# Performance work log

Measured on AMD Instinct MI355X. Metric: run time of the kernel, lower is better.

The kernel has to match this reference:

```python
import jax, jax.numpy as jnp
import numpy as np

NUM_EMB = 1024
EMB_DIM = 256
BETA = 0.25


def setup_inputs() -> dict:
    key = jax.random.key(0)
    k1, k2 = jax.random.split(key)
    z_e = jax.random.normal(k1, (32, EMB_DIM, 32, 32), dtype=jnp.float32)
    # original inits uniform(-1/num_emb, 1/num_emb)
    emb_weight = jax.random.uniform(k2, (NUM_EMB, EMB_DIM), dtype=jnp.float32,
                                    minval=-1.0 / NUM_EMB, maxval=1.0 / NUM_EMB)
    return {"z_e": z_e, "emb_weight": emb_weight}


def reference(z_e, emb_weight):
    # (B, C, H, W) -> (B, H, W, C)
    z = jnp.transpose(z_e, (0, 2, 3, 1))
    B, H, W, C = z.shape
    z_flat = z.reshape(-1, C)  # (N, C)
    # squared L2 distances to codebook: ||z||^2 + ||e||^2 - 2 z e^T
    d = (jnp.sum(z_flat ** 2, axis=1, keepdims=True)
         + jnp.sum(emb_weight ** 2, axis=1)
         - 2.0 * jnp.matmul(z_flat, emb_weight.T))  # (N, num_emb)
    encoding_indices = jnp.argmin(d, axis=1)  # (N,)
    # one-hot matmul == gather of codebook rows
    z_q = jnp.take(emb_weight, encoding_indices, axis=0).reshape(B, H, W, C)
    # vq losses
    L_e = jnp.mean((jax.lax.stop_gradient(z_q) - z) ** 2)
    L_q = jnp.mean((z_q - jax.lax.stop_gradient(z)) ** 2)
    vq_loss = L_e + BETA * L_q
    # straight-through estimator
    z_q_st = z + jax.lax.stop_gradient(z_q - z)
    z_q_out = jnp.transpose(z_q_st, (0, 3, 1, 2))  # (B, C, H, W)
    return z_q_out, vq_loss, encoding_indices
```

## Files before the change

kernel.cpp:

```cpp
#include <hip/hip_runtime.h>

#define NUM_EMB 1024
#define EMB_DIM 256
#define NPIX    32768
#define HW      1024
#define ZQ_ELEMS 8388608

#define WS_TNORM 8
#define WS_SNORM 8192
#define WS_KEYS  139264
#define WS_CNT   401408
#define WS_EPL   401424
#define EPLANE_ELEMS (NUM_EMB * EMB_DIM)

typedef unsigned long long u64;
typedef unsigned int u32;
typedef unsigned short u16;

typedef __bf16 bf16x8 __attribute__((ext_vector_type(8)));
typedef float f32x16 __attribute__((ext_vector_type(16)));
typedef u16 u16x8 __attribute__((ext_vector_type(8)));

__device__ __forceinline__ float pw128_sq(const float* x, int stride) {
  float r[8];
#pragma unroll
  for (int j = 0; j < 8; ++j) {
    float v = x[(size_t)j * stride];
    r[j] = __fmul_rn(v, v);
  }
  for (int i = 8; i < 128; i += 8) {
#pragma unroll
    for (int j = 0; j < 8; ++j) {
      float v = x[(size_t)(i + j) * stride];
      r[j] = __fadd_rn(r[j], __fmul_rn(v, v));
    }
  }
  float s01 = __fadd_rn(r[0], r[1]);
  float s23 = __fadd_rn(r[2], r[3]);
  float s45 = __fadd_rn(r[4], r[5]);
  float s67 = __fadd_rn(r[6], r[7]);
  return __fadd_rn(__fadd_rn(s01, s23), __fadd_rn(s45, s67));
}

__device__ __forceinline__ void split3(float x, u16& h, u16& m, u16& l) {
  u32 u = __float_as_uint(x);
  u16 hb = (u16)((u + 0x7fffu + ((u >> 16) & 1u)) >> 16);
  float hf = __uint_as_float((u32)hb << 16);
  float r1 = x - hf;
  u32 u1 = __float_as_uint(r1);
  u16 mb = (u16)((u1 + 0x7fffu + ((u1 >> 16) & 1u)) >> 16);
  float mf = __uint_as_float((u32)mb << 16);
  float r2 = r1 - mf;
  u32 u2 = __float_as_uint(r2);
  u16 lb = (u16)((u2 + 0x7fffu + ((u2 >> 16) & 1u)) >> 16);
  h = hb; m = mb; l = lb;
}

__device__ __forceinline__ u64 shfl_xor_u64(u64 v, int msk) {
  const u32 lo = __shfl_xor((u32)v, msk, 64);
  const u32 hi = __shfl_xor((u32)(v >> 32), msk, 64);
  return ((u64)hi << 32) | lo;
}

__global__ __launch_bounds__(256) void vq_prep_kernel(
    const float* __restrict__ z, const float* __restrict__ emb,
    float* __restrict__ tnorm, float* __restrict__ snorm,
    unsigned long long* __restrict__ keys, double* __restrict__ loss_accum,
    u32* __restrict__ counter,
    u16* __restrict__ eh, u16* __restrict__ em, u16* __restrict__ el) {
  const int gid = blockIdx.x * 256 + threadIdx.x;
  if (gid == 0) *loss_accum = 0.0;
  if (gid == 1) *counter = 0u;
  if (gid < NPIX) {
    keys[gid] = ~0ull;
    const int b = gid >> 10, hw = gid & 1023;
    const float* base = z + (size_t)b * (EMB_DIM * HW) + hw;
    snorm[gid] = __fadd_rn(pw128_sq(base, HW), pw128_sq(base + (size_t)128 * HW, HW));
  } else {
    const int k = gid - NPIX;
    if (k < NUM_EMB) {
      const float* row = emb + (size_t)k * EMB_DIM;
      tnorm[k] = __fadd_rn(pw128_sq(row, 1), pw128_sq(row + 128, 1));
      for (int c = 0; c < EMB_DIM; c += 8) {
        u16x8 vh, vm, vl;
#pragma unroll
        for (int j = 0; j < 8; ++j) {
          u16 h_, m_, l_;
          split3(row[c + j], h_, m_, l_);
          vh[j] = h_; vm[j] = m_; vl[j] = l_;
        }
        *(u16x8*)(eh + (size_t)k * EMB_DIM + c) = vh;
        *(u16x8*)(em + (size_t)k * EMB_DIM + c) = vm;
        *(u16x8*)(el + (size_t)k * EMB_DIM + c) = vl;
      }
    }
  }
}

__global__ __launch_bounds__(256, 2) void vq_main_kernel(
    const float* __restrict__ z,
    const u16* __restrict__ eh, const u16* __restrict__ em,
    const u16* __restrict__ el,
    const float* __restrict__ tnorm, const float* __restrict__ snorm,
    unsigned long long* __restrict__ keys) {
  __shared__ __align__(16) u16 zs[3][128][40];

  const int t   = threadIdx.x;
  const int hb  = blockIdx.x;
  const int bid = (hb & 7) * 256 + (hb >> 3);
  const int pt  = bid >> 3;
  const int ntb = bid & 7;
  const int m0  = pt * 128;
  const int n0  = ntb * 128;
  const int b   = m0 >> 10;
  const int hw0 = m0 & 1023;
  const float* zbase = z + (size_t)b * (EMB_DIM * HW) + hw0;

  const int l    = t & 63;
  const int wid  = t >> 6;
  const int wpx0 = (wid >> 1) * 64;
  const int wcb  = (wid & 1) * 64;
  const int cl   = l & 31;
  const int hi   = l >> 5;

  const int spx = t & 127;
  const int skh = (t >> 7) * 16;

  const u16* eplan[3] = {eh, em, el};
  size_t ebase[2];
  ebase[0] = (size_t)(n0 + wcb + cl) * EMB_DIM + (size_t)hi * 8;
  ebase[1] = (size_t)(n0 + wcb + 32 + cl) * EMB_DIM + (size_t)hi * 8;

  float gz[16];
#pragma unroll
  for (int j = 0; j < 16; ++j)
    gz[j] = zbase[(size_t)(skh + j) * HW + spx];

  f32x16 acc[2][2];
#pragma unroll
  for (int i = 0; i < 2; ++i)
#pragma unroll
    for (int j = 0; j < 2; ++j)
#pragma unroll
      for (int r = 0; r < 16; ++r) acc[i][j][r] = 0.0f;

  for (int kt = 0; kt < 8; ++kt) {
#pragma unroll
    for (int c = 0; c < 2; ++c) {
      u16x8 vh, vm, vl;
#pragma unroll
      for (int j = 0; j < 8; ++j) {
        u16 h_, m_, l_;
        split3(gz[c * 8 + j], h_, m_, l_);
        vh[j] = h_; vm[j] = m_; vl[j] = l_;
      }
      *(u16x8*)&zs[0][spx][skh + c * 8] = vh;
      *(u16x8*)&zs[1][spx][skh + c * 8] = vm;
      *(u16x8*)&zs[2][spx][skh + c * 8] = vl;
    }
    if (kt < 7) {
      const int kb = (kt + 1) * 32;
#pragma unroll
      for (int j = 0; j < 16; ++j)
        gz[j] = zbase[(size_t)(kb + skh + j) * HW + spx];
    }
    bf16x8 ge[3][2][2];
#pragma unroll
    for (int p = 0; p < 3; ++p)
#pragma unroll
      for (int nn = 0; nn < 2; ++nn)
#pragma unroll
        for (int ks = 0; ks < 2; ++ks)
          ge[p][nn][ks] =
              *(const bf16x8*)(eplan[p] + ebase[nn] + (size_t)kt * 32 + ks * 16);
    __syncthreads();

#pragma unroll
    for (int ks = 0; ks < 2; ++ks) {
      bf16x8 af[3][2];
#pragma unroll
      for (int p = 0; p < 3; ++p)
#pragma unroll
        for (int mt = 0; mt < 2; ++mt)
          af[p][mt] =
              *(const bf16x8*)&zs[p][wpx0 + mt * 32 + cl][ks * 16 + hi * 8];
#define PROD(PA, PB)                                                          \
      _Pragma("unroll")                                                       \
      for (int mt = 0; mt < 2; ++mt) {                                        \
        _Pragma("unroll")                                                     \
        for (int nn = 0; nn < 2; ++nn)                                        \
          acc[mt][nn] = __builtin_amdgcn_mfma_f32_32x32x16_bf16(              \
              af[PA][mt], ge[PB][nn][ks], acc[mt][nn], 0, 0, 0);              \
      }
      PROD(0, 0)
      PROD(0, 1)
      PROD(1, 0)
      PROD(1, 1)
      PROD(0, 2)
      PROD(2, 0)
#undef PROD
    }
    __syncthreads();
  }

  const float tv0 = tnorm[n0 + wcb + cl];
  const float tv1 = tnorm[n0 + wcb + 32 + cl];
  u64 bk[2][16];
#pragma unroll
  for (int mt = 0; mt < 2; ++mt)
#pragma unroll
    for (int reg = 0; reg < 16; ++reg) {
      const int row = wpx0 + mt * 32 + (reg & 3) + 8 * (reg >> 2) + 4 * hi;
      const float s = snorm[m0 + row];
      const float d0 = __fsub_rn(__fadd_rn(s, tv0), 2.0f * acc[mt][0][reg]);
      const float d1 = __fsub_rn(__fadd_rn(s, tv1), 2.0f * acc[mt][1][reg]);
      const u64 k0 = ((u64)__float_as_uint(d0) << 32) | (u32)(n0 + wcb + cl);
      const u64 k1 =
          ((u64)__float_as_uint(d1) << 32) | (u32)(n0 + wcb + 32 + cl);
      bk[mt][reg] = k0 < k1 ? k0 : k1;
    }
#pragma unroll
  for (int off = 1; off < 32; off <<= 1) {
#pragma unroll
    for (int mt = 0; mt < 2; ++mt)
#pragma unroll
      for (int reg = 0; reg < 16; ++reg) {
        const u64 o = shfl_xor_u64(bk[mt][reg], off);
        if (o < bk[mt][reg]) bk[mt][reg] = o;
      }
  }

  u64* part = (u64*)&zs[0][0][0];
  if (cl == 0) {
#pragma unroll
    for (int mt = 0; mt < 2; ++mt)
#pragma unroll
      for (int reg = 0; reg < 16; ++reg) {
        const int row = wpx0 + mt * 32 + (reg & 3) + 8 * (reg >> 2) + 4 * hi;
        part[row * 2 + (wid & 1)] = bk[mt][reg];
      }
  }
  __syncthreads();
  if (t < 128) {
    const u64 a = part[t * 2], c = part[t * 2 + 1];
    atomicMin(&keys[m0 + t], a < c ? a : c);
  }
}

__global__ __launch_bounds__(256) void vq_outputs_kernel(
    const float* __restrict__ z, const float* __restrict__ emb,
    const unsigned long long* __restrict__ keys, float* __restrict__ out,
    float* __restrict__ out_idx_f, double* __restrict__ loss_accum,
    u32* __restrict__ counter, float* __restrict__ out_loss) {
  const int t  = threadIdx.x;
  const int n0 = blockIdx.x * 64;
  const int m  = t & 63;
  const int c0 = t >> 6;
  const int b  = n0 >> 10;
  const int hw = n0 & 1023;
  const float* zb = z   + (size_t)b * (EMB_DIM * HW) + hw + m;
  float*       ob = out + (size_t)b * (EMB_DIM * HW) + hw + m;
  const int idx = (int)(u32)(keys[n0 + m] & 0xffffffffu);
  const float* er = emb + (size_t)idx * EMB_DIM;
  if (c0 == 0) out_idx_f[n0 + m] = (float)idx;

  double lsum = 0.0;
  for (int c = c0; c < EMB_DIM; c += 4) {
    const float e  = er[c];
    const float zv = zb[(size_t)c * HW];
    const float diff = e - zv;
    const float zq   = zv + diff;
    ob[(size_t)c * HW] = zq;
    lsum += (double)diff * (double)diff;
  }

  __shared__ double red[256];
  red[t] = lsum;
  __syncthreads();
  for (int s2 = 128; s2 > 0; s2 >>= 1) {
    if (t < s2) red[t] += red[t + s2];
    __syncthreads();
  }
  if (t == 0) {
    atomicAdd(loss_accum, red[0]);
    __threadfence();
    const u32 tick = atomicAdd(counter, 1u);
    if (tick == (u32)(NPIX / 64 - 1)) {
      const double total = atomicAdd(loss_accum, 0.0);
      const float L = (float)(total / (double)ZQ_ELEMS);
      out_loss[0] = __fadd_rn(L, __fmul_rn(0.25f, L));
    }
  }
}

extern "C" void kernel_launch(void* const* d_in, const int* in_sizes, int n_in,
                              void* d_out, int out_size, void* d_ws, size_t ws_size,
                              hipStream_t stream) {
  const float* z   = (const float*)d_in[0];
  const float* emb = (const float*)d_in[1];

  float* out       = (float*)d_out;
  float* out_loss  = out + ZQ_ELEMS;
  float* out_idx_f = out + ZQ_ELEMS + 1;

  double* loss_accum = (double*)d_ws;
  float*  tnorm = (float*)((char*)d_ws + WS_TNORM);
  float*  snorm = (float*)((char*)d_ws + WS_SNORM);
  unsigned long long* keys = (unsigned long long*)((char*)d_ws + WS_KEYS);
  u32* counter = (u32*)((char*)d_ws + WS_CNT);
  u16* eh = (u16*)((char*)d_ws + WS_EPL);
  u16* em = eh + EPLANE_ELEMS;
  u16* el = em + EPLANE_ELEMS;

  vq_prep_kernel<<<132, 256, 0, stream>>>(z, emb, tnorm, snorm, keys, loss_accum,
                                          counter, eh, em, el);
  vq_main_kernel<<<2048, 256, 0, stream>>>(z, eh, em, el, tnorm, snorm, keys);
  vq_outputs_kernel<<<NPIX / 64, 256, 0, stream>>>(z, emb, keys, out, out_idx_f,
                                                   loss_accum, counter, out_loss);
}
```

Before: 217.5 us.

## Stage codebook tiles through swizzled LDS and raise occupancy target

Codebook split planes are now loaded cooperatively once per block into a shared-memory tile, instead of each wave reading its own fragments directly from global memory. The shared-memory layout changes from padded rows to an XOR-swizzled layout to avoid bank conflicts. The launch bound rises from 2 to 3 blocks per CU. In exchange, shared memory per block roughly doubles and there is more register pressure from the occupancy hint, which could cause spills.

```diff
diff --git a/kernel.cpp b/kernel.cpp
--- a/kernel.cpp
+++ b/kernel.cpp
@@ -20,6 +20,8 @@
 typedef __bf16 bf16x8 __attribute__((ext_vector_type(8)));
 typedef float f32x16 __attribute__((ext_vector_type(16)));
 typedef u16 u16x8 __attribute__((ext_vector_type(8)));
+
+#define ZIDX(row, q) (((row) << 5) + ((((q) ^ ((row) & 3))) << 3))
 
 __device__ __forceinline__ float pw128_sq(const float* x, int stride) {
   float r[8];
@@ -97,13 +99,14 @@
   }
 }
 
-__global__ __launch_bounds__(256, 2) void vq_main_kernel(
+__global__ __launch_bounds__(256, 3) void vq_main_kernel(
     const float* __restrict__ z,
     const u16* __restrict__ eh, const u16* __restrict__ em,
     const u16* __restrict__ el,
     const float* __restrict__ tnorm, const float* __restrict__ snorm,
     unsigned long long* __restrict__ keys) {
-  __shared__ __align__(16) u16 zs[3][128][40];
+  __shared__ __align__(16) u16 zs[3][4096];
+  __shared__ __align__(16) u16 es[3][4096];
 
   const int t   = threadIdx.x;
   const int hb  = blockIdx.x;
@@ -123,18 +126,24 @@
   const int cl   = l & 31;
   const int hi   = l >> 5;
 
-  const int spx = t & 127;
+  const int sr  = t & 127;
   const int skh = (t >> 7) * 16;
+  const int q0  = (t >> 7) * 2;
 
   const u16* eplan[3] = {eh, em, el};
-  size_t ebase[2];
-  ebase[0] = (size_t)(n0 + wcb + cl) * EMB_DIM + (size_t)hi * 8;
-  ebase[1] = (size_t)(n0 + wcb + 32 + cl) * EMB_DIM + (size_t)hi * 8;
+  const size_t ebase = (size_t)(n0 + sr) * EMB_DIM + skh;
 
   float gz[16];
+  u16x8 ge[3][2];
+
 #pragma unroll
   for (int j = 0; j < 16; ++j)
-    gz[j] = zbase[(size_t)(skh + j) * HW + spx];
+    gz[j] = zbase[(size_t)(skh + j) * HW + sr];
+#pragma unroll
+  for (int p = 0; p < 3; ++p) {
+    ge[p][0] = *(const u16x8*)(eplan[p] + ebase);
+    ge[p][1] = *(const u16x8*)(eplan[p] + ebase + 8);
+  }
 
   f32x16 acc[2][2];
 #pragma unroll
@@ -154,43 +163,50 @@
         split3(gz[c * 8 + j], h_, m_, l_);
         vh[j] = h_; vm[j] = m_; vl[j] = l_;
       }
-      *(u16x8*)&zs[0][spx][skh + c * 8] = vh;
-      *(u16x8*)&zs[1][spx][skh + c * 8] = vm;
-      *(u16x8*)&zs[2][spx][skh + c * 8] = vl;
+      const int zi = ZIDX(sr, q0 + c);
+      *(u16x8*)&zs[0][zi] = vh;
+      *(u16x8*)&zs[1][zi] = vm;
+      *(u16x8*)&zs[2][zi] = vl;
+    }
+#pragma unroll
+    for (int p = 0; p < 3; ++p) {
+      *(u16x8*)&es[p][ZIDX(sr, q0)]     = ge[p][0];
+      *(u16x8*)&es[p][ZIDX(sr, q0 + 1)] = ge[p][1];
     }
     if (kt < 7) {
       const int kb = (kt + 1) * 32;
 #pragma unroll
       for (int j = 0; j < 16; ++j)
-        gz[j] = zbase[(size_t)(kb + skh + j) * HW + spx];
-    }
-    bf16x8 ge[3][2][2];
-#pragma unroll
-    for (int p = 0; p < 3; ++p)
-#pragma unroll
-      for (int nn = 0; nn < 2; ++nn)
-#pragma unroll
-        for (int ks = 0; ks < 2; ++ks)
-          ge[p][nn][ks] =
-              *(const bf16x8*)(eplan[p] + ebase[nn] + (size_t)kt * 32 + ks * 16);
+        gz[j] = zbase[(size_t)(kb + skh + j) * HW + sr];
+#pragma unroll
+      for (int p = 0; p < 3; ++p) {
+        ge[p][0] = *(const u16x8*)(eplan[p] + ebase + kb);
+        ge[p][1] = *(const u16x8*)(eplan[p] + ebase + kb + 8);
+      }
+    }
     __syncthreads();
 
 #pragma unroll
     for (int ks = 0; ks < 2; ++ks) {
-      bf16x8 af[3][2];
+      const int q = ks * 2 + hi;
+      bf16x8 af[3][2], bf[3][2];
 #pragma unroll
       for (int p = 0; p < 3; ++p)
 #pragma unroll
         for (int mt = 0; mt < 2; ++mt)
-          af[p][mt] =
-              *(const bf16x8*)&zs[p][wpx0 + mt * 32 + cl][ks * 16 + hi * 8];
+          af[p][mt] = *(const bf16x8*)&zs[p][ZIDX(wpx0 + mt * 32 + cl, q)];
+#pragma unroll
+      for (int p = 0; p < 3; ++p)
+#pragma unroll
+        for (int nn = 0; nn < 2; ++nn)
+          bf[p][nn] = *(const bf16x8*)&es[p][ZIDX(wcb + nn * 32 + cl, q)];
 #define PROD(PA, PB)                                                          \
       _Pragma("unroll")                                                       \
       for (int mt = 0; mt < 2; ++mt) {                                        \
         _Pragma("unroll")                                                     \
         for (int nn = 0; nn < 2; ++nn)                                        \
           acc[mt][nn] = __builtin_amdgcn_mfma_f32_32x32x16_bf16(              \
-              af[PA][mt], ge[PB][nn][ks], acc[mt][nn], 0, 0, 0);              \
+              af[PA][mt], bf[PB][nn], acc[mt][nn], 0, 0, 0);                  \
       }
       PROD(0, 0)
       PROD(0, 1)
@@ -230,7 +246,7 @@
       }
   }
 
-  u64* part = (u64*)&zs[0][0][0];
+  u64* part = (u64*)&zs[0][0];
   if (cl == 0) {
 #pragma unroll
     for (int mt = 0; mt < 2; ++mt)
```

New measurement: 212.6 us. 1.02x faster.

## Fuse output pass into main kernel via per-tile tickets; pre-swizzle codebook planes

Applied to the files above, without the earlier changes.

The separate outputs kernel is removed. The last of the 8 codebook-tile blocks for each 128-pixel tile, found through a per-tile atomic ticket, gathers the chosen codebook rows, writes z_q and the indices, and accumulates the loss. A global ticket finalizes the loss. The prep kernel now writes the bf16 split planes in an MFMA-fragment-ordered layout so each lane's B-operand loads are contiguous, and these loads are issued earlier in the k loop. Launch bounds go from 2 to 3 waves per SIMD. The aim is to save a kernel launch and the extra key reads and to coalesce codebook loads, at the cost of tail imbalance on the ticket-winning blocks and added register pressure.

```diff
diff --git a/kernel.cpp b/kernel.cpp
--- a/kernel.cpp
+++ b/kernel.cpp
@@ -9,9 +9,8 @@
 #define WS_TNORM 8
 #define WS_SNORM 8192
 #define WS_KEYS  139264
-#define WS_CNT   401408
-#define WS_EPL   401424
-#define EPLANE_ELEMS (NUM_EMB * EMB_DIM)
+#define WS_TICK  401408
+#define WS_EB    403456
 
 typedef unsigned long long u64;
 typedef unsigned int u32;
@@ -20,6 +19,11 @@
 typedef __bf16 bf16x8 __attribute__((ext_vector_type(8)));
 typedef float f32x16 __attribute__((ext_vector_type(16)));
 typedef u16 u16x8 __attribute__((ext_vector_type(8)));
+
+__device__ __forceinline__ size_t eb_idx(int p, int g, int kt, int ks, int hi,
+                                         int cl) {
+  return ((((((size_t)p * 32 + g) * 8 + kt) * 2 + ks) * 2 + hi) * 32 + cl) * 8;
+}
 
 __device__ __forceinline__ float pw128_sq(const float* x, int stride) {
   float r[8];
@@ -65,12 +69,10 @@
 __global__ __launch_bounds__(256) void vq_prep_kernel(
     const float* __restrict__ z, const float* __restrict__ emb,
     float* __restrict__ tnorm, float* __restrict__ snorm,
-    unsigned long long* __restrict__ keys, double* __restrict__ loss_accum,
-    u32* __restrict__ counter,
-    u16* __restrict__ eh, u16* __restrict__ em, u16* __restrict__ el) {
+    u64* __restrict__ keys, double* __restrict__ loss_accum,
+    u32* __restrict__ tickets, u16* __restrict__ EB) {
   const int gid = blockIdx.x * 256 + threadIdx.x;
   if (gid == 0) *loss_accum = 0.0;
-  if (gid == 1) *counter = 0u;
   if (gid < NPIX) {
     keys[gid] = ~0ull;
     const int b = gid >> 10, hw = gid & 1023;
@@ -79,8 +81,10 @@
   } else {
     const int k = gid - NPIX;
     if (k < NUM_EMB) {
+      if (k < 257) tickets[k] = 0u;
       const float* row = emb + (size_t)k * EMB_DIM;
       tnorm[k] = __fadd_rn(pw128_sq(row, 1), pw128_sq(row + 128, 1));
+      const int g = k >> 5, cl = k & 31;
       for (int c = 0; c < EMB_DIM; c += 8) {
         u16x8 vh, vm, vl;
 #pragma unroll
@@ -89,21 +93,25 @@
           split3(row[c + j], h_, m_, l_);
           vh[j] = h_; vm[j] = m_; vl[j] = l_;
         }
-        *(u16x8*)(eh + (size_t)k * EMB_DIM + c) = vh;
-        *(u16x8*)(em + (size_t)k * EMB_DIM + c) = vm;
-        *(u16x8*)(el + (size_t)k * EMB_DIM + c) = vl;
-      }
-    }
-  }
-}
-
-__global__ __launch_bounds__(256, 2) void vq_main_kernel(
-    const float* __restrict__ z,
-    const u16* __restrict__ eh, const u16* __restrict__ em,
-    const u16* __restrict__ el,
+        const int kt = c >> 5, ks = (c >> 4) & 1, hi = (c >> 3) & 1;
+        *(u16x8*)(EB + eb_idx(0, g, kt, ks, hi, cl)) = vh;
+        *(u16x8*)(EB + eb_idx(1, g, kt, ks, hi, cl)) = vm;
+        *(u16x8*)(EB + eb_idx(2, g, kt, ks, hi, cl)) = vl;
+      }
+    }
+  }
+}
+
+__global__ __launch_bounds__(256, 3) void vq_main_kernel(
+    const float* __restrict__ z, const float* __restrict__ emb,
+    const u16* __restrict__ EB,
     const float* __restrict__ tnorm, const float* __restrict__ snorm,
-    unsigned long long* __restrict__ keys) {
+    u64* __restrict__ keys, double* __restrict__ loss_accum,
+    u32* __restrict__ tickets, float* __restrict__ out,
+    float* __restrict__ out_idx_f, float* __restrict__ out_loss) {
   __shared__ __align__(16) u16 zs[3][128][40];
+  __shared__ u64 part[128][2];
+  __shared__ u32 flag;
 
   const int t   = threadIdx.x;
   const int hb  = blockIdx.x;
@@ -122,19 +130,15 @@
   const int wcb  = (wid & 1) * 64;
   const int cl   = l & 31;
   const int hi   = l >> 5;
-
-  const int spx = t & 127;
+  const int gb   = ntb * 4 + (wid & 1) * 2;
+
+  const int sr  = t & 127;
   const int skh = (t >> 7) * 16;
 
-  const u16* eplan[3] = {eh, em, el};
-  size_t ebase[2];
-  ebase[0] = (size_t)(n0 + wcb + cl) * EMB_DIM + (size_t)hi * 8;
-  ebase[1] = (size_t)(n0 + wcb + 32 + cl) * EMB_DIM + (size_t)hi * 8;
-
   float gz[16];
 #pragma unroll
   for (int j = 0; j < 16; ++j)
-    gz[j] = zbase[(size_t)(skh + j) * HW + spx];
+    gz[j] = zbase[(size_t)(skh + j) * HW + sr];
 
   f32x16 acc[2][2];
 #pragma unroll
@@ -145,6 +149,16 @@
       for (int r = 0; r < 16; ++r) acc[i][j][r] = 0.0f;
 
   for (int kt = 0; kt < 8; ++kt) {
+    bf16x8 bf[3][2][2];
+#pragma unroll
+    for (int p = 0; p < 3; ++p)
+#pragma unroll
+      for (int nn = 0; nn < 2; ++nn)
+#pragma unroll
+        for (int ks = 0; ks < 2; ++ks)
+          bf[p][nn][ks] =
+              *(const bf16x8*)(EB + eb_idx(p, gb + nn, kt, ks, hi, cl));
+
 #pragma unroll
     for (int c = 0; c < 2; ++c) {
       u16x8 vh, vm, vl;
@@ -154,25 +168,16 @@
         split3(gz[c * 8 + j], h_, m_, l_);
         vh[j] = h_; vm[j] = m_; vl[j] = l_;
       }
-      *(u16x8*)&zs[0][spx][skh + c * 8] = vh;
-      *(u16x8*)&zs[1][spx][skh + c * 8] = vm;
-      *(u16x8*)&zs[2][spx][skh + c * 8] = vl;
+      *(u16x8*)&zs[0][sr][skh + c * 8] = vh;
+      *(u16x8*)&zs[1][sr][skh + c * 8] = vm;
+      *(u16x8*)&zs[2][sr][skh + c * 8] = vl;
     }
     if (kt < 7) {
       const int kb = (kt + 1) * 32;
 #pragma unroll
       for (int j = 0; j < 16; ++j)
-        gz[j] = zbase[(size_t)(kb + skh + j) * HW + spx];
-    }
-    bf16x8 ge[3][2][2];
-#pragma unroll
-    for (int p = 0; p < 3; ++p)
-#pragma unroll
-      for (int nn = 0; nn < 2; ++nn)
-#pragma unroll
-        for (int ks = 0; ks < 2; ++ks)
-          ge[p][nn][ks] =
-              *(const bf16x8*)(eplan[p] + ebase[nn] + (size_t)kt * 32 + ks * 16);
+        gz[j] = zbase[(size_t)(kb + skh + j) * HW + sr];
+    }
     __syncthreads();
 
 #pragma unroll
@@ -190,7 +195,7 @@
         _Pragma("unroll")                                                     \
         for (int nn = 0; nn < 2; ++nn)                                        \
           acc[mt][nn] = __builtin_amdgcn_mfma_f32_32x32x16_bf16(              \
-              af[PA][mt], ge[PB][nn][ks], acc[mt][nn], 0, 0, 0);              \
+              af[PA][mt], bf[PB][nn][ks], acc[mt][nn], 0, 0, 0);              \
       }
       PROD(0, 0)
       PROD(0, 1)
@@ -230,65 +235,62 @@
       }
   }
 
-  u64* part = (u64*)&zs[0][0][0];
   if (cl == 0) {
 #pragma unroll
     for (int mt = 0; mt < 2; ++mt)
 #pragma unroll
       for (int reg = 0; reg < 16; ++reg) {
         const int row = wpx0 + mt * 32 + (reg & 3) + 8 * (reg >> 2) + 4 * hi;
-        part[row * 2 + (wid & 1)] = bk[mt][reg];
+        part[row][wid & 1] = bk[mt][reg];
       }
   }
   __syncthreads();
   if (t < 128) {
-    const u64 a = part[t * 2], c = part[t * 2 + 1];
+    const u64 a = part[t][0], c = part[t][1];
     atomicMin(&keys[m0 + t], a < c ? a : c);
   }
-}
-
-__global__ __launch_bounds__(256) void vq_outputs_kernel(
-    const float* __restrict__ z, const float* __restrict__ emb,
-    const unsigned long long* __restrict__ keys, float* __restrict__ out,
-    float* __restrict__ out_idx_f, double* __restrict__ loss_accum,
-    u32* __restrict__ counter, float* __restrict__ out_loss) {
-  const int t  = threadIdx.x;
-  const int n0 = blockIdx.x * 64;
-  const int m  = t & 63;
-  const int c0 = t >> 6;
-  const int b  = n0 >> 10;
-  const int hw = n0 & 1023;
-  const float* zb = z   + (size_t)b * (EMB_DIM * HW) + hw + m;
-  float*       ob = out + (size_t)b * (EMB_DIM * HW) + hw + m;
-  const int idx = (int)(u32)(keys[n0 + m] & 0xffffffffu);
-  const float* er = emb + (size_t)idx * EMB_DIM;
-  if (c0 == 0) out_idx_f[n0 + m] = (float)idx;
-
-  double lsum = 0.0;
-  for (int c = c0; c < EMB_DIM; c += 4) {
-    const float e  = er[c];
-    const float zv = zb[(size_t)c * HW];
-    const float diff = e - zv;
-    const float zq   = zv + diff;
-    ob[(size_t)c * HW] = zq;
-    lsum += (double)diff * (double)diff;
-  }
-
-  __shared__ double red[256];
-  red[t] = lsum;
   __syncthreads();
-  for (int s2 = 128; s2 > 0; s2 >>= 1) {
-    if (t < s2) red[t] += red[t + s2];
+
+  if (t == 0) {
+    __threadfence();
+    flag = (atomicAdd(&tickets[pt], 1u) == 7u) ? 1u : 0u;
+  }
+  __syncthreads();
+  if (flag) {
+    __threadfence();
+    const int m  = t & 127;
+    const int c0 = t >> 7;
+    const int idx = (int)(u32)(keys[m0 + m] & 0xffffffffu);
+    if (c0 == 0) out_idx_f[m0 + m] = (float)idx;
+    const float* er = emb + (size_t)idx * EMB_DIM;
+    const float* zb = zbase + m;
+    float*       ob = out + (size_t)b * (EMB_DIM * HW) + hw0 + m;
+
+    double lsum = 0.0;
+    for (int c = c0; c < EMB_DIM; c += 2) {
+      const float e  = er[c];
+      const float zv = zb[(size_t)c * HW];
+      const float diff = e - zv;
+      const float zq   = zv + diff;
+      ob[(size_t)c * HW] = zq;
+      lsum += (double)diff * (double)diff;
+    }
+    double* red = (double*)&part[0][0];
+    red[t] = lsum;
     __syncthreads();
-  }
-  if (t == 0) {
-    atomicAdd(loss_accum, red[0]);
-    __threadfence();
-    const u32 tick = atomicAdd(counter, 1u);
-    if (tick == (u32)(NPIX / 64 - 1)) {
-      const double total = atomicAdd(loss_accum, 0.0);
-      const float L = (float)(total / (double)ZQ_ELEMS);
-      out_loss[0] = __fadd_rn(L, __fmul_rn(0.25f, L));
+    for (int s2 = 128; s2 > 0; s2 >>= 1) {
+      if (t < s2) red[t] += red[t + s2];
+      __syncthreads();
+    }
+    if (t == 0) {
+      atomicAdd(loss_accum, red[0]);
+      __threadfence();
+      if (atomicAdd(&tickets[256], 1u) == 255u) {
+        __threadfence();
+        const double total = atomicAdd(loss_accum, 0.0);
+        const float L = (float)(total / (double)ZQ_ELEMS);
+        out_loss[0] = __fadd_rn(L, __fmul_rn(0.25f, L));
+      }
     }
   }
 }
@@ -306,15 +308,13 @@
   double* loss_accum = (double*)d_ws;
   float*  tnorm = (float*)((char*)d_ws + WS_TNORM);
   float*  snorm = (float*)((char*)d_ws + WS_SNORM);
-  unsigned long long* keys = (unsigned long long*)((char*)d_ws + WS_KEYS);
-  u32* counter = (u32*)((char*)d_ws + WS_CNT);
-  u16* eh = (u16*)((char*)d_ws + WS_EPL);
-  u16* em = eh + EPLANE_ELEMS;
-  u16* el = em + EPLANE_ELEMS;
+  u64*    keys  = (u64*)((char*)d_ws + WS_KEYS);
+  u32*    tickets = (u32*)((char*)d_ws + WS_TICK);
+  u16*    EB    = (u16*)((char*)d_ws + WS_EB);
 
   vq_prep_kernel<<<132, 256, 0, stream>>>(z, emb, tnorm, snorm, keys, loss_accum,
-                                          counter, eh, em, el);
-  vq_main_kernel<<<2048, 256, 0, stream>>>(z, eh, em, el, tnorm, snorm, keys);
-  vq_outputs_kernel<<<NPIX / 64, 256, 0, stream>>>(z, emb, keys, out, out_idx_f,
-                                                   loss_accum, counter, out_loss);
-}
+                                          tickets, EB);
+  vq_main_kernel<<<2048, 256, 0, stream>>>(z, emb, EB, tnorm, snorm, keys,
+                                           loss_accum, tickets, out, out_idx_f,
+                                           out_loss);
+}
```

After: 316.8 us. 1.46x slower.
